# Kernel optimization log

Measured on AMD Instinct MI355X. Metric: run time of the kernel, lower is better.

The kernel has to match this reference:

```python
import jax, jax.numpy as jnp
import numpy as np

B, N, C, H, DFF = 4, 1024, 768, 12, 3072
D = C // H
EPS = 1e-5


def _layernorm(x, w, b, axes):
    mu = jnp.mean(x, axis=axes, keepdims=True)
    var = jnp.mean(jnp.square(x - mu), axis=axes, keepdims=True)
    return (x - mu) * jax.lax.rsqrt(var + EPS) * w + b


def setup_inputs() -> dict:
    key = jax.random.key(0)
    ks = jax.random.split(key, 8)
    s = lambda fan_in: 1.0 / np.sqrt(fan_in)
    return {
        'x': jax.random.normal(ks[0], (B, N, C), jnp.float32),
        'ln0_w': jnp.ones((C,), jnp.float32),
        'ln0_b': jnp.zeros((C,), jnp.float32),
        'qkv_w': jax.random.normal(ks[1], (3 * C, C), jnp.float32) * s(C),
        'qkv_b': jax.random.normal(ks[2], (3 * C,), jnp.float32) * 0.01,
        'proj_w': jax.random.normal(ks[3], (C, C), jnp.float32) * s(C),
        'proj_b': jax.random.normal(ks[4], (C,), jnp.float32) * 0.01,
        'attn_norm_w': jnp.ones((H, N, N), jnp.float32),
        'attn_norm_b': jnp.zeros((H, N, N), jnp.float32),
        'ln1_w': jnp.ones((C,), jnp.float32),
        'ln1_b': jnp.zeros((C,), jnp.float32),
        'fc1_w': jax.random.normal(ks[5], (DFF, C), jnp.float32) * s(C),
        'fc1_b': jax.random.normal(ks[6], (DFF,), jnp.float32) * 0.01,
        'fc2_w': jax.random.normal(ks[7], (C, DFF), jnp.float32) * s(DFF),
        'fc2_b': jnp.zeros((C,), jnp.float32),
    }


def reference(x, ln0_w, ln0_b, qkv_w, qkv_b, proj_w, proj_b,
              attn_norm_w, attn_norm_b, ln1_w, ln1_b,
              fc1_w, fc1_b, fc2_w, fc2_b):
    # pre-norm
    h = _layernorm(x, ln0_w, ln0_b, axes=-1)
    # qkv projection -> (3, B, H, N, D)
    qkv = (h @ qkv_w.T + qkv_b).reshape(B, N, 3, H, D).transpose(2, 0, 3, 1, 4)
    q, k, v = qkv[0], qkv[1], qkv[2]
    # grassmanian_point: project each head vector onto the unit sphere
    q = q / jnp.linalg.norm(q, axis=-1, keepdims=True)
    k = k / jnp.linalg.norm(k, axis=-1, keepdims=True)
    # sum_d (q_{id} k_{jd})^2  ==  (q^2) @ (k^2)^T   -- avoids (B,H,D,N,N) tensor
    attn = jnp.einsum('bhid,bhjd->bhij', jnp.square(q), jnp.square(k))
    # LayerNorm over (H, N, N) jointly per batch element
    attn = _layernorm(attn, attn_norm_w, attn_norm_b, axes=(1, 2, 3))
    out = jnp.einsum('bhij,bhjd->bhid', attn, v)
    out = out.transpose(0, 2, 1, 3).reshape(B, N, C)
    out = out @ proj_w.T + proj_b
    # residual + post-norm + FFN (dropout/drop_path are identity in eval)
    src = x + out
    src = _layernorm(src, ln1_w, ln1_b, axes=-1)
    ff = jax.nn.gelu(src @ fc1_w.T + fc1_b, approximate=False) @ fc2_w.T + fc2_b
    src = src + ff
    return src, attn
```

## Files before the change

kernel.cpp:

```cpp
#include <hip/hip_runtime.h>

typedef __bf16 bf16;
typedef __bf16 bf16x4 __attribute__((ext_vector_type(4)));
typedef __bf16 bf16x8 __attribute__((ext_vector_type(8)));
typedef float f32x4 __attribute__((ext_vector_type(4)));

#define DEVI __device__ __forceinline__

typedef const __attribute__((address_space(1))) void* gas1;
typedef __attribute__((address_space(3))) void* las3;

DEVI int xcd_chunk(int bid, int nwg)
{
  const int q = nwg >> 3, r = nwg & 7;
  const int xcd = bid & 7, rank = bid >> 3;
  return (xcd < r) ? xcd * (q + 1) + rank
                   : r * (q + 1) + (xcd - r) * q + rank;
}

DEVI void stage_tile(const bf16* g, int ld, char* lds, int bytes, int tid)
{
  const int wv = tid >> 6, lane = tid & 63;
  const char* gb = (const char*)g;
  const long rowb = (long)ld * 2;
  for (int off = wv * 1024; off < bytes; off += 4096) {
    const int o  = off + lane * 16;
    const int s  = o ^ (((o >> 7) & 7) << 4);
    const int r  = s >> 7;
    const int cb = s & 127;
    __builtin_amdgcn_global_load_lds((gas1)(gb + (long)r * rowb + cb),
                                     (las3)(lds + off), 16, 0, 0);
  }
}

template<int N> DEVI void waitvm()
{
  if constexpr (N == 8)      asm volatile("s_waitcnt vmcnt(8)" ::: "memory");
  else if constexpr (N == 6) asm volatile("s_waitcnt vmcnt(6)" ::: "memory");
  else if constexpr (N == 4) asm volatile("s_waitcnt vmcnt(4)" ::: "memory");
  else if constexpr (N == 2) asm volatile("s_waitcnt vmcnt(2)" ::: "memory");
  else                       asm volatile("s_waitcnt vmcnt(0)" ::: "memory");
}

DEVI void wave_lds_fence()
{
  asm volatile("s_waitcnt lgkmcnt(0)" ::: "memory");
  __builtin_amdgcn_sched_barrier(0);
}

struct EpiQKV {
  const float* bias; bf16* C;
  DEVI void operator()(int z, int row, int col, float v) const {
    C[(long)row * 2304 + col] = (bf16)(v + bias[col]);
  }
};

struct EpiProj {
  const float* bias; const float* x; float* src;
  DEVI void operator()(int z, int row, int col, float v) const {
    const long i = (long)row * 768 + col;
    src[i] = v + bias[col] + x[i];
  }
};

struct EpiGelu {
  const float* bias; bf16* g;
  DEVI void operator()(int z, int row, int col, float v) const {
    const float t = v + bias[col];
    const float r = 0.5f * t * (1.0f + erff(t * 0.70710678118654752f));
    g[(long)row * 3072 + col] = (bf16)r;
  }
};

struct EpiOut {
  const float* bias; const float* lnf; float* outp;
  DEVI void operator()(int z, int row, int col, float v) const {
    const long i = (long)row * 768 + col;
    outp[i] = v + bias[col] + lnf[i];
  }
};

template<int BM, int BN, int WC, int FM, int FN, int WPE, class Epi>
__global__ __launch_bounds__(256, WPE) void gemm_k(
    const bf16* __restrict__ A, long abatch,
    const bf16* __restrict__ B, long bbatch,
    int lda, int ldb, int K, Epi epi)
{
  constexpr int BK = 64;
  constexpr int AB = BM * BK * 2, BB = BN * BK * 2;
  constexpr int BUFB = AB + BB;
  constexpr int LPS = BUFB / 4096;
  __shared__ char smem[2 * BUFB];

  const int tid = threadIdx.x, lane = tid & 63, wv = tid >> 6;
  const int wr = wv / WC, wc = wv % WC;
  const int NT = gridDim.x;
  const int nwg = NT * gridDim.y;
  const int wid = xcd_chunk(blockIdx.y * NT + blockIdx.x, nwg);
  const int mt = wid / NT, nt = wid % NT;
  const int z = blockIdx.z;
  const long abase = (long)z * abatch + (long)mt * BM * lda;
  const long bbase = (long)z * bbatch + (long)nt * BN * ldb;
  const int l15 = lane & 15;
  const int sw = (lane & 7) << 4;

  auto stage_all = [&](int buf, int kt) {
    char* base = smem + buf * BUFB;
    stage_tile(A + abase + kt, lda, base, AB, tid);
    stage_tile(B + bbase + kt, ldb, base + AB, BB, tid);
  };

  f32x4 acc[FM][FN];
#pragma unroll
  for (int m = 0; m < FM; ++m)
#pragma unroll
    for (int n = 0; n < FN; ++n) acc[m][n] = f32x4{0.f, 0.f, 0.f, 0.f};

  const int arow = wr * FM * 16, bcol = wc * FN * 16;
  const int T = K / BK;

  stage_all(0, 0);
  int cur = 0;
  for (int t = 0; t < T; ++t) {
    if (t + 1 < T) { stage_all(cur ^ 1, (t + 1) * BK); waitvm<LPS>(); }
    else           { waitvm<0>(); }
    __builtin_amdgcn_s_barrier();
    asm volatile("" ::: "memory");

    const char* As = smem + cur * BUFB;
    const char* Bs = As + AB;
#pragma unroll
    for (int ks = 0; ks < 2; ++ks) {
      const int ko = (ks * 64 + (lane >> 4) * 16) ^ sw;
      bf16x8 av[FM], bv[FN];
#pragma unroll
      for (int m = 0; m < FM; ++m)
        av[m] = *(const bf16x8*)(As + (arow + m * 16 + l15) * 128 + ko);
#pragma unroll
      for (int n = 0; n < FN; ++n)
        bv[n] = *(const bf16x8*)(Bs + (bcol + n * 16 + l15) * 128 + ko);
#pragma unroll
      for (int m = 0; m < FM; ++m)
#pragma unroll
        for (int n = 0; n < FN; ++n)
          acc[m][n] = __builtin_amdgcn_mfma_f32_16x16x32_bf16(av[m], bv[n], acc[m][n], 0, 0, 0);
    }
    asm volatile("s_waitcnt lgkmcnt(0)" ::: "memory");
    __builtin_amdgcn_s_barrier();
    asm volatile("" ::: "memory");
    cur ^= 1;
  }

#pragma unroll
  for (int m = 0; m < FM; ++m)
#pragma unroll
    for (int n = 0; n < FN; ++n)
#pragma unroll
      for (int r = 0; r < 4; ++r) {
        const int grow = mt * BM + arow + m * 16 + (lane >> 4) * 4 + r;
        const int gcol = nt * BN + bcol + n * 16 + l15;
        epi(z, grow, gcol, acc[m][n][r]);
      }
}

__global__ __launch_bounds__(256, 3) void attn_fused(
    const bf16* __restrict__ q2h, const bf16* __restrict__ k2h,
    const bf16* __restrict__ vth, const float* __restrict__ stats,
    const float* __restrict__ wn, const float* __restrict__ bn,
    float* __restrict__ attn_out, bf16* __restrict__ oh)
{
  __shared__ char smem[49152];
  char* Qs  = smem;
  char* Ks0 = smem + 8192;
  char* Ks1 = smem + 16384;
  char* Vs0 = smem + 24576;
  char* Vs1 = smem + 32768;
  char* Pall = smem + 40960;

  const int tid = threadIdx.x, lane = tid & 63, wv = tid >> 6;
  const int wid = xcd_chunk(blockIdx.x, 768);
  const int b = wid & 3;
  const int mt = (wid >> 2) & 15;
  const int h = wid >> 6;
  const int zq = b * 12 + h;
  const float mu = stats[2 * b], rs = stats[2 * b + 1];
  const int l15 = lane & 15, lhi = lane >> 4;
  const int sw = (lane & 7) << 4;
  char* Ps = Pall + wv * 2048;

  const long zoff = (long)zq * 65536;
  stage_tile(q2h + zoff + (long)mt * 4096, 64, Qs, 8192, tid);
  stage_tile(k2h + zoff, 64, Ks0, 8192, tid);
  stage_tile(vth + zoff, 1024, Vs0, 8192, tid);
  __syncthreads();

  f32x4 oacc[4];
#pragma unroll
  for (int n = 0; n < 4; ++n) oacc[n] = f32x4{0.f, 0.f, 0.f, 0.f};

  for (int nt = 0; nt < 16; ++nt) {
    const int cur = nt & 1;
    char* Kc = cur ? Ks1 : Ks0;
    char* Vc = cur ? Vs1 : Vs0;
    char* Kn = cur ? Ks0 : Ks1;
    char* Vn = cur ? Vs0 : Vs1;

    if (nt + 1 < 16) {
      stage_tile(k2h + zoff + (long)(nt + 1) * 4096, 64, Kn, 8192, tid);
      stage_tile(vth + zoff + (nt + 1) * 64, 1024, Vn, 8192, tid);
    }
    f32x4 wreg[4], breg[4];
#pragma unroll
    for (int rr = 0; rr < 4; ++rr) {
      const long grow = (long)mt * 64 + wv * 16 + rr * 4 + lhi;
      const long gcol = (long)nt * 64 + l15 * 4;
      wreg[rr] = *(const f32x4*)&wn[((long)h * 1024 + grow) * 1024 + gcol];
      breg[rr] = *(const f32x4*)&bn[((long)h * 1024 + grow) * 1024 + gcol];
    }

    f32x4 acc[4];
#pragma unroll
    for (int n = 0; n < 4; ++n) acc[n] = f32x4{0.f, 0.f, 0.f, 0.f};
    __builtin_amdgcn_s_setprio(1);
#pragma unroll
    for (int ks = 0; ks < 2; ++ks) {
      const int ko = (ks * 64 + lhi * 16) ^ sw;
      const bf16x8 av = *(const bf16x8*)(Qs + (wv * 16 + l15) * 128 + ko);
#pragma unroll
      for (int n = 0; n < 4; ++n) {
        const bf16x8 bv = *(const bf16x8*)(Kc + (n * 16 + l15) * 128 + ko);
        acc[n] = __builtin_amdgcn_mfma_f32_16x16x32_bf16(av, bv, acc[n], 0, 0, 0);
      }
    }
    __builtin_amdgcn_s_setprio(0);
#pragma unroll
    for (int n = 0; n < 4; ++n)
#pragma unroll
      for (int r = 0; r < 4; ++r) {
        const int row = lhi * 4 + r;
        const int cb = (n * 32 + l15 * 2) ^ ((row & 7) << 4);
        *(bf16*)(Ps + row * 128 + cb) = (bf16)((acc[n][r] - mu) * rs);
      }
    wave_lds_fence();

#pragma unroll
    for (int rr = 0; rr < 4; ++rr) {
      const int row = rr * 4 + lhi;
      const int cb = (l15 * 8) ^ ((row & 7) << 4);
      const bf16x4 s4 = *(const bf16x4*)(Ps + row * 128 + cb);
      const long grow = (long)mt * 64 + wv * 16 + row;
      const long gcol = (long)nt * 64 + l15 * 4;
      f32x4 r4;
      bf16x4 h4;
#pragma unroll
      for (int e = 0; e < 4; ++e) {
        const float r = (float)s4[e] * wreg[rr][e] + breg[rr][e];
        r4[e] = r;
        h4[e] = (bf16)r;
      }
      *(f32x4*)&attn_out[((long)zq * 1024 + grow) * 1024 + gcol] = r4;
      *(bf16x4*)(Ps + row * 128 + cb) = h4;
    }
    wave_lds_fence();

    __builtin_amdgcn_s_setprio(1);
#pragma unroll
    for (int ks = 0; ks < 2; ++ks) {
      const int ko = (ks * 64 + lhi * 16) ^ sw;
      const bf16x8 av = *(const bf16x8*)(Ps + l15 * 128 + ko);
#pragma unroll
      for (int n = 0; n < 4; ++n) {
        const bf16x8 bv = *(const bf16x8*)(Vc + (n * 16 + l15) * 128 + ko);
        oacc[n] = __builtin_amdgcn_mfma_f32_16x16x32_bf16(av, bv, oacc[n], 0, 0, 0);
      }
    }
    __builtin_amdgcn_s_setprio(0);
    __syncthreads();
  }

#pragma unroll
  for (int n = 0; n < 4; ++n)
#pragma unroll
    for (int r = 0; r < 4; ++r) {
      const int row = mt * 64 + wv * 16 + lhi * 4 + r;
      const int col = n * 16 + l15;
      oh[((long)(b * 1024 + row)) * 768 + h * 64 + col] = (bf16)oacc[n][r];
    }
}

__global__ void cast_bf16(const float* __restrict__ s, bf16* __restrict__ d, int n4)
{
  const int i = blockIdx.x * 256 + threadIdx.x;
  if (i < n4) {
    const f32x4 v = *(const f32x4*)&s[i * 4];
    bf16x4 o;
#pragma unroll
    for (int j = 0; j < 4; ++j) o[j] = (bf16)v[j];
    *(bf16x4*)&d[i * 4] = o;
  }
}

__global__ __launch_bounds__(256) void ln_row(
    const float* __restrict__ in, const float* __restrict__ w,
    const float* __restrict__ b, bf16* __restrict__ outh,
    float* __restrict__ outf)
{
  __shared__ float red[256];
  const int row = blockIdx.x, tid = threadIdx.x;
  const float* p = in + (long)row * 768;
  const float v0 = p[tid], v1 = p[tid + 256], v2 = p[tid + 512];
  red[tid] = v0 + v1 + v2;
  __syncthreads();
  for (int st = 128; st > 0; st >>= 1) { if (tid < st) red[tid] += red[tid + st]; __syncthreads(); }
  const float mu = red[0] * (1.0f / 768.0f);
  __syncthreads();
  const float d0 = v0 - mu, d1 = v1 - mu, d2 = v2 - mu;
  red[tid] = d0 * d0 + d1 * d1 + d2 * d2;
  __syncthreads();
  for (int st = 128; st > 0; st >>= 1) { if (tid < st) red[tid] += red[tid + st]; __syncthreads(); }
  const float rs = rsqrtf(red[0] * (1.0f / 768.0f) + 1e-5f);
  const float dv[3] = {d0, d1, d2};
#pragma unroll
  for (int k = 0; k < 3; ++k) {
    const int c = tid + k * 256;
    const float h = dv[k] * rs * w[c] + b[c];
    outh[(long)row * 768 + c] = (bf16)h;
    if (outf) outf[(long)row * 768 + c] = h;
  }
}

__global__ __launch_bounds__(256) void qkv_post(
    const bf16* __restrict__ qkv, bf16* __restrict__ q2h,
    bf16* __restrict__ k2h, bf16* __restrict__ vb)
{
  const int row = blockIdx.x;
  const int b = row >> 10, n = row & 1023;
  const int sg = threadIdx.x >> 3, l8 = threadIdx.x & 7;
  for (int t = sg; t < 36; t += 32) {
    const int s = t / 12, h = t - s * 12;
    const bf16x8 v8 = *(const bf16x8*)&qkv[(long)row * 2304 + s * 768 + h * 64 + l8 * 8];
    const long addr = (((long)(b * 12 + h)) * 1024 + n) * 64 + l8 * 8;
    if (s == 2) {
      *(bf16x8*)&vb[addr] = v8;
    } else {
      float f[8];
      float sq = 0.f;
#pragma unroll
      for (int e = 0; e < 8; ++e) { f[e] = (float)v8[e]; sq += f[e] * f[e]; }
      float tot = sq;
      tot += __shfl_xor(tot, 1);
      tot += __shfl_xor(tot, 2);
      tot += __shfl_xor(tot, 4);
      const float inv = 1.0f / tot;
      bf16x8 o;
#pragma unroll
      for (int e = 0; e < 8; ++e) o[e] = (bf16)(f[e] * f[e] * inv);
      if (s == 0) *(bf16x8*)&q2h[addr] = o;
      else        *(bf16x8*)&k2h[addr] = o;
    }
  }
}

__global__ __launch_bounds__(256) void transpose_v(
    const bf16* __restrict__ vb, bf16* __restrict__ vth)
{
  __shared__ float t[64][65];
  const int z = blockIdx.y, n0 = blockIdx.x * 64, tid = threadIdx.x;
  const bf16* srcp = vb + ((long)z * 1024 + n0) * 64;
  for (int e = tid * 8; e < 4096; e += 2048) {
    const bf16x8 v8 = *(const bf16x8*)&srcp[e];
    const int r = e >> 6, c = e & 63;
#pragma unroll
    for (int j = 0; j < 8; ++j) t[r][c + j] = (float)v8[j];
  }
  __syncthreads();
  for (int e = tid; e < 512; e += 256) {
    const int d = e >> 3, c0 = (e & 7) * 8;
    bf16x8 o;
#pragma unroll
    for (int j = 0; j < 8; ++j) o[j] = (bf16)t[c0 + j][d];
    *(bf16x8*)&vth[((long)z * 64 + d) * 1024 + n0 + c0] = o;
  }
}

__global__ __launch_bounds__(256) void stats_accum(
    const bf16* __restrict__ q2h, const bf16* __restrict__ k2h,
    float* __restrict__ Gq, float* __restrict__ Gk,
    float* __restrict__ Sq, float* __restrict__ Sk)
{
  __shared__ float rowbuf[8][128];
  const int tid = threadIdx.x;
  const int z = blockIdx.y;
  const long base = ((long)z * 1024 + (long)blockIdx.x * 128) * 64;
  const int tx = tid & 15, ty = tid >> 4;
  float gq[4][4] = {}, gk[4][4] = {};
  float sq = 0.f, sk = 0.f;
  for (int r0 = 0; r0 < 128; r0 += 8) {
    __syncthreads();
    {
      const int idx = tid * 4;
      const int rr = idx >> 7, cc = idx & 127;
      const long a = base + (long)(r0 + rr) * 64 + (cc & 63);
      const bf16x4 v4 = (cc < 64) ? *(const bf16x4*)&q2h[a]
                                  : *(const bf16x4*)&k2h[a];
#pragma unroll
      for (int j = 0; j < 4; ++j) rowbuf[rr][cc + j] = (float)v4[j];
    }
    __syncthreads();
#pragma unroll
    for (int r = 0; r < 8; ++r) {
      float qa[4], qe[4], ka[4], ke[4];
#pragma unroll
      for (int i = 0; i < 4; ++i) {
        qa[i] = rowbuf[r][ty * 4 + i]; qe[i] = rowbuf[r][tx * 4 + i];
        ka[i] = rowbuf[r][64 + ty * 4 + i]; ke[i] = rowbuf[r][64 + tx * 4 + i];
      }
#pragma unroll
      for (int i = 0; i < 4; ++i)
#pragma unroll
        for (int j = 0; j < 4; ++j) {
          gq[i][j] += qa[i] * qe[j];
          gk[i][j] += ka[i] * ke[j];
        }
    }
    if (tid < 128) {
      float s = 0.f;
#pragma unroll
      for (int r = 0; r < 8; ++r) s += rowbuf[r][tid];
      if (tid < 64) sq += s; else sk += s;
    }
  }
#pragma unroll
  for (int i = 0; i < 4; ++i)
#pragma unroll
    for (int j = 0; j < 4; ++j) {
      atomicAdd(&Gq[(long)z * 4096 + (ty * 4 + i) * 64 + tx * 4 + j], gq[i][j]);
      atomicAdd(&Gk[(long)z * 4096 + (ty * 4 + i) * 64 + tx * 4 + j], gk[i][j]);
    }
  if (tid < 64) atomicAdd(&Sq[z * 64 + tid], sq);
  else if (tid < 128) atomicAdd(&Sk[z * 64 + tid - 64], sk);
}

__global__ __launch_bounds__(256) void stats_final(
    const float* __restrict__ Gq, const float* __restrict__ Gk,
    const float* __restrict__ Sq, const float* __restrict__ Sk,
    float* __restrict__ stats)
{
  __shared__ double red[256];
  const int b = blockIdx.x, tid = threadIdx.x;
  double s2 = 0.0, s1 = 0.0;
  for (int h = 0; h < 12; ++h) {
    const float* gq = Gq + ((long)(b * 12 + h)) * 4096;
    const float* gk = Gk + ((long)(b * 12 + h)) * 4096;
    for (int i = tid; i < 4096; i += 256) s2 += (double)gq[i] * (double)gk[i];
    const float* sqp = Sq + (b * 12 + h) * 64;
    const float* skp = Sk + (b * 12 + h) * 64;
    for (int i = tid; i < 64; i += 256) s1 += (double)sqp[i] * (double)skp[i];
  }
  red[tid] = s2; __syncthreads();
  for (int st = 128; st > 0; st >>= 1) { if (tid < st) red[tid] += red[tid + st]; __syncthreads(); }
  const double S2 = red[0]; __syncthreads();
  red[tid] = s1; __syncthreads();
  for (int st = 128; st > 0; st >>= 1) { if (tid < st) red[tid] += red[tid + st]; __syncthreads(); }
  if (tid == 0) {
    const double S1 = red[0];
    const double cnt = 12.0 * 1024.0 * 1024.0;
    const double mean = S1 / cnt;
    const double var = S2 / cnt - mean * mean;
    stats[2 * b] = (float)mean;
    stats[2 * b + 1] = (float)(1.0 / sqrt(var + 1e-5));
  }
}

extern "C" void kernel_launch(void* const* d_in, const int* in_sizes, int n_in,
                              void* d_out, int out_size, void* d_ws, size_t ws_size,
                              hipStream_t stream)
{
  const float* x      = (const float*)d_in[0];
  const float* ln0_w  = (const float*)d_in[1];
  const float* ln0_b  = (const float*)d_in[2];
  const float* qkv_w  = (const float*)d_in[3];
  const float* qkv_b  = (const float*)d_in[4];
  const float* proj_w = (const float*)d_in[5];
  const float* proj_b = (const float*)d_in[6];
  const float* attn_w = (const float*)d_in[7];
  const float* attn_b = (const float*)d_in[8];
  const float* ln1_w  = (const float*)d_in[9];
  const float* ln1_b  = (const float*)d_in[10];
  const float* fc1_w  = (const float*)d_in[11];
  const float* fc1_b  = (const float*)d_in[12];
  const float* fc2_w  = (const float*)d_in[13];
  const float* fc2_b  = (const float*)d_in[14];

  float* out_src  = (float*)d_out;
  float* out_attn = out_src + 4L * 1024 * 768;

  char* p = (char*)d_ws;
  auto take = [&](long bytes) -> char* {
    char* r = p;
    p += (bytes + 255) & ~255L;
    return r;
  };
  bf16* qkvw_h = (bf16*)take(3538944);
  bf16* projw_h = (bf16*)take(1179648);
  bf16* fc1w_h = (bf16*)take(4718592);
  bf16* fc2w_h = (bf16*)take(4718592);
  char* regB = take(12582912);
  bf16* hh = (bf16*)regB;
  float* src = (float*)regB;
  char* regC = take(37748736);
  bf16* qkvb = (bf16*)regC;
  bf16* gact = (bf16*)regC;
  float* ln1f = (float*)(regC + 25165824);
  bf16* q2h = (bf16*)take(6291456);
  bf16* k2h = (bf16*)take(6291456);
  bf16* vb  = (bf16*)take(6291456);
  bf16* vth = (bf16*)take(6291456);
  bf16* oh  = (bf16*)take(6291456);
  bf16* h1v = (bf16*)take(6291456);
  float* Gq = (float*)take(786432);
  float* Gk = (float*)take(786432);
  float* Sq = (float*)take(12288);
  float* Sk = (float*)take(12288);
  float* stats = (float*)take(256);

  const dim3 blk(256);

  (void)hipMemsetAsync((void*)Gq, 0, 786432 * 2 + 12288 * 2 + 256, stream);

  cast_bf16<<<dim3(1769472 / 4 / 256), blk, 0, stream>>>(qkv_w, qkvw_h, 442368);
  cast_bf16<<<dim3(589824 / 4 / 256), blk, 0, stream>>>(proj_w, projw_h, 147456);
  cast_bf16<<<dim3(2359296 / 4 / 256), blk, 0, stream>>>(fc1_w, fc1w_h, 589824);
  cast_bf16<<<dim3(2359296 / 4 / 256), blk, 0, stream>>>(fc2_w, fc2w_h, 589824);

  ln_row<<<dim3(4096), blk, 0, stream>>>(x, ln0_w, ln0_b, hh, nullptr);

  gemm_k<128, 64, 2, 4, 2, 3, EpiQKV><<<dim3(36, 32, 1), blk, 0, stream>>>(
      hh, 0, qkvw_h, 0, 768, 768, 768, EpiQKV{qkv_b, qkvb});

  qkv_post<<<dim3(4096), blk, 0, stream>>>(qkvb, q2h, k2h, vb);
  transpose_v<<<dim3(16, 48), blk, 0, stream>>>(vb, vth);
  stats_accum<<<dim3(8, 48), blk, 0, stream>>>(q2h, k2h, Gq, Gk, Sq, Sk);
  stats_final<<<dim3(4), blk, 0, stream>>>(Gq, Gk, Sq, Sk, stats);

  attn_fused<<<dim3(768), blk, 0, stream>>>(
      q2h, k2h, vth, stats, attn_w, attn_b, out_attn, oh);

  gemm_k<128, 64, 2, 4, 2, 3, EpiProj><<<dim3(12, 32, 1), blk, 0, stream>>>(
      oh, 0, projw_h, 0, 768, 768, 768, EpiProj{proj_b, x, src});

  ln_row<<<dim3(4096), blk, 0, stream>>>(src, ln1_w, ln1_b, h1v, ln1f);

  gemm_k<128, 64, 2, 4, 2, 3, EpiGelu><<<dim3(48, 32, 1), blk, 0, stream>>>(
      h1v, 0, fc1w_h, 0, 768, 768, 768, EpiGelu{fc1_b, gact});

  gemm_k<128, 64, 2, 4, 2, 3, EpiOut><<<dim3(12, 32, 1), blk, 0, stream>>>(
      gact, 0, fc2w_h, 0, 3072, 3072, 3072, EpiOut{fc2_b, ln1f, out_src});
}
```

Measured before the change: 384.3 us.

## Read K/V directly from global in attention, drop LDS staging; fuse weight casts

```diff
diff --git a/kernel.cpp b/kernel.cpp
--- a/kernel.cpp
+++ b/kernel.cpp
@@ -163,19 +163,15 @@
       }
 }
 
-__global__ __launch_bounds__(256, 3) void attn_fused(
+__global__ __launch_bounds__(256, 4) void attn_fused(
     const bf16* __restrict__ q2h, const bf16* __restrict__ k2h,
     const bf16* __restrict__ vth, const float* __restrict__ stats,
     const float* __restrict__ wn, const float* __restrict__ bn,
     float* __restrict__ attn_out, bf16* __restrict__ oh)
 {
-  __shared__ char smem[49152];
-  char* Qs  = smem;
-  char* Ks0 = smem + 8192;
-  char* Ks1 = smem + 16384;
-  char* Vs0 = smem + 24576;
-  char* Vs1 = smem + 32768;
-  char* Pall = smem + 40960;
+  __shared__ char smem[16384];
+  char* Qs   = smem;
+  char* Pall = smem + 8192;
 
   const int tid = threadIdx.x, lane = tid & 63, wv = tid >> 6;
   const int wid = xcd_chunk(blockIdx.x, 768);
@@ -190,8 +186,6 @@
 
   const long zoff = (long)zq * 65536;
   stage_tile(q2h + zoff + (long)mt * 4096, 64, Qs, 8192, tid);
-  stage_tile(k2h + zoff, 64, Ks0, 8192, tid);
-  stage_tile(vth + zoff, 1024, Vs0, 8192, tid);
   __syncthreads();
 
   f32x4 oacc[4];
@@ -199,16 +193,6 @@
   for (int n = 0; n < 4; ++n) oacc[n] = f32x4{0.f, 0.f, 0.f, 0.f};
 
   for (int nt = 0; nt < 16; ++nt) {
-    const int cur = nt & 1;
-    char* Kc = cur ? Ks1 : Ks0;
-    char* Vc = cur ? Vs1 : Vs0;
-    char* Kn = cur ? Ks0 : Ks1;
-    char* Vn = cur ? Vs0 : Vs1;
-
-    if (nt + 1 < 16) {
-      stage_tile(k2h + zoff + (long)(nt + 1) * 4096, 64, Kn, 8192, tid);
-      stage_tile(vth + zoff + (nt + 1) * 64, 1024, Vn, 8192, tid);
-    }
     f32x4 wreg[4], breg[4];
 #pragma unroll
     for (int rr = 0; rr < 4; ++rr) {
@@ -226,9 +210,11 @@
     for (int ks = 0; ks < 2; ++ks) {
       const int ko = (ks * 64 + lhi * 16) ^ sw;
       const bf16x8 av = *(const bf16x8*)(Qs + (wv * 16 + l15) * 128 + ko);
+      const int ke = ks * 32 + lhi * 8;
 #pragma unroll
       for (int n = 0; n < 4; ++n) {
-        const bf16x8 bv = *(const bf16x8*)(Kc + (n * 16 + l15) * 128 + ko);
+        const bf16x8 bv =
+            *(const bf16x8*)&k2h[zoff + (long)(nt * 64 + n * 16 + l15) * 64 + ke];
         acc[n] = __builtin_amdgcn_mfma_f32_16x16x32_bf16(av, bv, acc[n], 0, 0, 0);
       }
     }
@@ -268,14 +254,16 @@
     for (int ks = 0; ks < 2; ++ks) {
       const int ko = (ks * 64 + lhi * 16) ^ sw;
       const bf16x8 av = *(const bf16x8*)(Ps + l15 * 128 + ko);
+      const int ke = nt * 64 + ks * 32 + lhi * 8;
 #pragma unroll
       for (int n = 0; n < 4; ++n) {
-        const bf16x8 bv = *(const bf16x8*)(Vc + (n * 16 + l15) * 128 + ko);
+        const bf16x8 bv =
+            *(const bf16x8*)&vth[zoff + (long)(n * 16 + l15) * 1024 + ke];
         oacc[n] = __builtin_amdgcn_mfma_f32_16x16x32_bf16(av, bv, oacc[n], 0, 0, 0);
       }
     }
     __builtin_amdgcn_s_setprio(0);
-    __syncthreads();
+    wave_lds_fence();
   }
 
 #pragma unroll
@@ -288,16 +276,22 @@
     }
 }
 
-__global__ void cast_bf16(const float* __restrict__ s, bf16* __restrict__ d, int n4)
+__global__ void cast_all(const float* __restrict__ qkvw, const float* __restrict__ projw,
+                         const float* __restrict__ fc1w, const float* __restrict__ fc2w,
+                         bf16* __restrict__ dq, bf16* __restrict__ dp,
+                         bf16* __restrict__ d1, bf16* __restrict__ d2)
 {
   const int i = blockIdx.x * 256 + threadIdx.x;
-  if (i < n4) {
-    const f32x4 v = *(const f32x4*)&s[i * 4];
-    bf16x4 o;
-#pragma unroll
-    for (int j = 0; j < 4; ++j) o[j] = (bf16)v[j];
-    *(bf16x4*)&d[i * 4] = o;
-  }
+  const float* s; bf16* d; int off;
+  if (i < 442368)       { s = qkvw; d = dq; off = i; }
+  else if (i < 589824)  { s = projw; d = dp; off = i - 442368; }
+  else if (i < 1179648) { s = fc1w; d = d1; off = i - 589824; }
+  else                  { s = fc2w; d = d2; off = i - 1179648; }
+  const f32x4 v = *(const f32x4*)&s[(long)off * 4];
+  bf16x4 o;
+#pragma unroll
+  for (int j = 0; j < 4; ++j) o[j] = (bf16)v[j];
+  *(bf16x4*)&d[(long)off * 4] = o;
 }
 
 __global__ __launch_bounds__(256) void ln_row(
@@ -528,10 +522,8 @@
 
   (void)hipMemsetAsync((void*)Gq, 0, 786432 * 2 + 12288 * 2 + 256, stream);
 
-  cast_bf16<<<dim3(1769472 / 4 / 256), blk, 0, stream>>>(qkv_w, qkvw_h, 442368);
-  cast_bf16<<<dim3(589824 / 4 / 256), blk, 0, stream>>>(proj_w, projw_h, 147456);
-  cast_bf16<<<dim3(2359296 / 4 / 256), blk, 0, stream>>>(fc1_w, fc1w_h, 589824);
-  cast_bf16<<<dim3(2359296 / 4 / 256), blk, 0, stream>>>(fc2_w, fc2w_h, 589824);
+  cast_all<<<dim3(1769472 / 256), blk, 0, stream>>>(
+      qkv_w, proj_w, fc1_w, fc2_w, qkvw_h, projw_h, fc1w_h, fc2w_h);
 
   ln_row<<<dim3(4096), blk, 0, stream>>>(x, ln0_w, ln0_b, hh, nullptr);
 
```

New measurement: 434.7 us. +13.1%, slower.

## Fuse QKV post-processing into QKV GEMM epilogue and merge weight casts

Applied to the files above, without the earlier changes.

```diff
diff --git a/kernel.cpp b/kernel.cpp
--- a/kernel.cpp
+++ b/kernel.cpp
@@ -47,13 +47,6 @@
   asm volatile("s_waitcnt lgkmcnt(0)" ::: "memory");
   __builtin_amdgcn_sched_barrier(0);
 }
-
-struct EpiQKV {
-  const float* bias; bf16* C;
-  DEVI void operator()(int z, int row, int col, float v) const {
-    C[(long)row * 2304 + col] = (bf16)(v + bias[col]);
-  }
-};
 
 struct EpiProj {
   const float* bias; const float* x; float* src;
@@ -163,6 +156,128 @@
       }
 }
 
+__global__ __launch_bounds__(256, 3) void gemm_qkv(
+    const bf16* __restrict__ A, const bf16* __restrict__ B,
+    const float* __restrict__ bias, bf16* __restrict__ q2h,
+    bf16* __restrict__ k2h, bf16* __restrict__ vb)
+{
+  constexpr int BM = 128, BN = 64, BK = 64;
+  constexpr int AB = BM * BK * 2, BB = BN * BK * 2;
+  constexpr int BUFB = AB + BB;
+  constexpr int LPS = BUFB / 4096;
+  __shared__ char smem[2 * BUFB];
+  __shared__ float rowsum[2][BM];
+
+  const int tid = threadIdx.x, lane = tid & 63, wv = tid >> 6;
+  const int wr = wv >> 1, wc = wv & 1;
+  const int NT = 36;
+  const int wid = xcd_chunk(blockIdx.y * NT + blockIdx.x, NT * 32);
+  const int mt = wid / NT, nt = wid % NT;
+  const int sec = nt / 12, h = nt - sec * 12;
+  const long abase = (long)mt * BM * 768;
+  const long bbase = (long)nt * BN * 768;
+  const int l15 = lane & 15, lhi = lane >> 4;
+  const int sw = (lane & 7) << 4;
+
+  auto stage_all = [&](int buf, int kt) {
+    char* base = smem + buf * BUFB;
+    stage_tile(A + abase + kt, 768, base, AB, tid);
+    stage_tile(B + bbase + kt, 768, base + AB, BB, tid);
+  };
+
+  f32x4 acc[4][2];
+#pragma unroll
+  for (int m = 0; m < 4; ++m)
+#pragma unroll
+    for (int n = 0; n < 2; ++n) acc[m][n] = f32x4{0.f, 0.f, 0.f, 0.f};
+
+  const int arow = wr * 64, bcol = wc * 32;
+
+  stage_all(0, 0);
+  int cur = 0;
+  for (int t = 0; t < 12; ++t) {
+    if (t + 1 < 12) { stage_all(cur ^ 1, (t + 1) * BK); waitvm<LPS>(); }
+    else            { waitvm<0>(); }
+    __builtin_amdgcn_s_barrier();
+    asm volatile("" ::: "memory");
+
+    const char* As = smem + cur * BUFB;
+    const char* Bs = As + AB;
+#pragma unroll
+    for (int ks = 0; ks < 2; ++ks) {
+      const int ko = (ks * 64 + lhi * 16) ^ sw;
+      bf16x8 av[4], bv[2];
+#pragma unroll
+      for (int m = 0; m < 4; ++m)
+        av[m] = *(const bf16x8*)(As + (arow + m * 16 + l15) * 128 + ko);
+#pragma unroll
+      for (int n = 0; n < 2; ++n)
+        bv[n] = *(const bf16x8*)(Bs + (bcol + n * 16 + l15) * 128 + ko);
+#pragma unroll
+      for (int m = 0; m < 4; ++m)
+#pragma unroll
+        for (int n = 0; n < 2; ++n)
+          acc[m][n] = __builtin_amdgcn_mfma_f32_16x16x32_bf16(av[m], bv[n], acc[m][n], 0, 0, 0);
+    }
+    asm volatile("s_waitcnt lgkmcnt(0)" ::: "memory");
+    __builtin_amdgcn_s_barrier();
+    asm volatile("" ::: "memory");
+    cur ^= 1;
+  }
+
+  float val[4][2][4];
+#pragma unroll
+  for (int m = 0; m < 4; ++m)
+#pragma unroll
+    for (int n = 0; n < 2; ++n)
+#pragma unroll
+      for (int r = 0; r < 4; ++r)
+        val[m][n][r] = acc[m][n][r] + bias[nt * 64 + bcol + n * 16 + l15];
+
+  if (sec < 2) {
+#pragma unroll
+    for (int m = 0; m < 4; ++m)
+#pragma unroll
+      for (int r = 0; r < 4; ++r) {
+        float p = val[m][0][r] * val[m][0][r] + val[m][1][r] * val[m][1][r];
+        p += __shfl_xor(p, 1);
+        p += __shfl_xor(p, 2);
+        p += __shfl_xor(p, 4);
+        p += __shfl_xor(p, 8);
+        if (l15 == 0) rowsum[wc][arow + m * 16 + lhi * 4 + r] = p;
+      }
+    __syncthreads();
+    bf16* dst = (sec == 0) ? q2h : k2h;
+#pragma unroll
+    for (int m = 0; m < 4; ++m)
+#pragma unroll
+      for (int r = 0; r < 4; ++r) {
+        const int row = arow + m * 16 + lhi * 4 + r;
+        const float inv = 1.0f / (rowsum[0][row] + rowsum[1][row]);
+        const int grow = mt * BM + row;
+        const int b = grow >> 10, nn = grow & 1023;
+        const long base = (((long)(b * 12 + h)) * 1024 + nn) * 64;
+#pragma unroll
+        for (int n = 0; n < 2; ++n) {
+          const float v = val[m][n][r];
+          dst[base + bcol + n * 16 + l15] = (bf16)(v * v * inv);
+        }
+      }
+  } else {
+#pragma unroll
+    for (int m = 0; m < 4; ++m)
+#pragma unroll
+      for (int r = 0; r < 4; ++r) {
+        const int grow = mt * BM + arow + m * 16 + lhi * 4 + r;
+        const int b = grow >> 10, nn = grow & 1023;
+        const long base = (((long)(b * 12 + h)) * 1024 + nn) * 64;
+#pragma unroll
+        for (int n = 0; n < 2; ++n)
+          vb[base + bcol + n * 16 + l15] = (bf16)val[m][n][r];
+      }
+  }
+}
+
 __global__ __launch_bounds__(256, 3) void attn_fused(
     const bf16* __restrict__ q2h, const bf16* __restrict__ k2h,
     const bf16* __restrict__ vth, const float* __restrict__ stats,
@@ -288,16 +403,22 @@
     }
 }
 
-__global__ void cast_bf16(const float* __restrict__ s, bf16* __restrict__ d, int n4)
+__global__ void cast_all(const float* __restrict__ qkvw, const float* __restrict__ projw,
+                         const float* __restrict__ fc1w, const float* __restrict__ fc2w,
+                         bf16* __restrict__ dq, bf16* __restrict__ dp,
+                         bf16* __restrict__ d1, bf16* __restrict__ d2)
 {
   const int i = blockIdx.x * 256 + threadIdx.x;
-  if (i < n4) {
-    const f32x4 v = *(const f32x4*)&s[i * 4];
-    bf16x4 o;
-#pragma unroll
-    for (int j = 0; j < 4; ++j) o[j] = (bf16)v[j];
-    *(bf16x4*)&d[i * 4] = o;
-  }
+  const float* s; bf16* d; int off;
+  if (i < 442368)       { s = qkvw; d = dq; off = i; }
+  else if (i < 589824)  { s = projw; d = dp; off = i - 442368; }
+  else if (i < 1179648) { s = fc1w; d = d1; off = i - 589824; }
+  else                  { s = fc2w; d = d2; off = i - 1179648; }
+  const f32x4 v = *(const f32x4*)&s[(long)off * 4];
+  bf16x4 o;
+#pragma unroll
+  for (int j = 0; j < 4; ++j) o[j] = (bf16)v[j];
+  *(bf16x4*)&d[(long)off * 4] = o;
 }
 
 __global__ __launch_bounds__(256) void ln_row(
@@ -329,38 +450,6 @@
   }
 }
 
-__global__ __launch_bounds__(256) void qkv_post(
-    const bf16* __restrict__ qkv, bf16* __restrict__ q2h,
-    bf16* __restrict__ k2h, bf16* __restrict__ vb)
-{
-  const int row = blockIdx.x;
-  const int b = row >> 10, n = row & 1023;
-  const int sg = threadIdx.x >> 3, l8 = threadIdx.x & 7;
-  for (int t = sg; t < 36; t += 32) {
-    const int s = t / 12, h = t - s * 12;
-    const bf16x8 v8 = *(const bf16x8*)&qkv[(long)row * 2304 + s * 768 + h * 64 + l8 * 8];
-    const long addr = (((long)(b * 12 + h)) * 1024 + n) * 64 + l8 * 8;
-    if (s == 2) {
-      *(bf16x8*)&vb[addr] = v8;
-    } else {
-      float f[8];
-      float sq = 0.f;
-#pragma unroll
-      for (int e = 0; e < 8; ++e) { f[e] = (float)v8[e]; sq += f[e] * f[e]; }
-      float tot = sq;
-      tot += __shfl_xor(tot, 1);
-      tot += __shfl_xor(tot, 2);
-      tot += __shfl_xor(tot, 4);
-      const float inv = 1.0f / tot;
-      bf16x8 o;
-#pragma unroll
-      for (int e = 0; e < 8; ++e) o[e] = (bf16)(f[e] * f[e] * inv);
-      if (s == 0) *(bf16x8*)&q2h[addr] = o;
-      else        *(bf16x8*)&k2h[addr] = o;
-    }
-  }
-}
-
 __global__ __launch_bounds__(256) void transpose_v(
     const bf16* __restrict__ vb, bf16* __restrict__ vth)
 {
@@ -509,7 +598,6 @@
   bf16* hh = (bf16*)regB;
   float* src = (float*)regB;
   char* regC = take(37748736);
-  bf16* qkvb = (bf16*)regC;
   bf16* gact = (bf16*)regC;
   float* ln1f = (float*)(regC + 25165824);
   bf16* q2h = (bf16*)take(6291456);
@@ -528,17 +616,14 @@
 
   (void)hipMemsetAsync((void*)Gq, 0, 786432 * 2 + 12288 * 2 + 256, stream);
 
-  cast_bf16<<<dim3(1769472 / 4 / 256), blk, 0, stream>>>(qkv_w, qkvw_h, 442368);
-  cast_bf16<<<dim3(589824 / 4 / 256), blk, 0, stream>>>(proj_w, projw_h, 147456);
-  cast_bf16<<<dim3(2359296 / 4 / 256), blk, 0, stream>>>(fc1_w, fc1w_h, 589824);
-  cast_bf16<<<dim3(2359296 / 4 / 256), blk, 0, stream>>>(fc2_w, fc2w_h, 589824);
+  cast_all<<<dim3(1769472 / 256), blk, 0, stream>>>(
+      qkv_w, proj_w, fc1_w, fc2_w, qkvw_h, projw_h, fc1w_h, fc2w_h);
 
   ln_row<<<dim3(4096), blk, 0, stream>>>(x, ln0_w, ln0_b, hh, nullptr);
 
-  gemm_k<128, 64, 2, 4, 2, 3, EpiQKV><<<dim3(36, 32, 1), blk, 0, stream>>>(
-      hh, 0, qkvw_h, 0, 768, 768, 768, EpiQKV{qkv_b, qkvb});
-
-  qkv_post<<<dim3(4096), blk, 0, stream>>>(qkvb, q2h, k2h, vb);
+  gemm_qkv<<<dim3(36, 32), blk, 0, stream>>>(
+      hh, qkvw_h, qkv_b, q2h, k2h, vb);
+
   transpose_v<<<dim3(16, 48), blk, 0, stream>>>(vb, vth);
   stats_accum<<<dim3(8, 48), blk, 0, stream>>>(q2h, k2h, Gq, Gk, Sq, Sk);
   stats_final<<<dim3(4), blk, 0, stream>>>(Gq, Gk, Sq, Sk, stats);
```

After: 380.3 us. Within noise of the previous version (-1.0%).
